# Performance work log

Hardware: AMD Instinct MI355X
Metric: run time of the kernel (lower is better)

Reference implementation:

```python
import jax, jax.numpy as jnp
import numpy as np
from jax import lax

VOCAB = 32000; D = 1024; NL = 4; DI = 2048; S = 16; R = 64; DC = 4
B = 1; L = 1024; EPS = 1e-5


def setup_inputs() -> dict:
    key = jax.random.key(0)
    ks = jax.random.split(key, 16)
    def n(k, shape, s=0.02):
        return jax.random.normal(k, shape, dtype=jnp.float32) * s
    return dict(
        tokens=jax.random.randint(ks[0], (B, L), 0, VOCAB),
        embed=n(ks[1], (VOCAB, D)),
        norm_w=jnp.ones((NL, D), jnp.float32) + n(ks[2], (NL, D)),
        in_proj_w=n(ks[3], (NL, 2 * DI, D)),
        conv_w=n(ks[4], (NL, DI, DC), 0.1),
        conv_b=n(ks[5], (NL, DI)),
        x_proj_w=n(ks[6], (NL, R + 2 * S, DI)),
        dt_proj_w=n(ks[7], (NL, DI, R), 0.1),
        dt_proj_b=n(ks[8], (NL, DI), 0.5),
        A_log=n(ks[9], (NL, DI, S), 0.5),
        D_param=jnp.ones((NL, DI), jnp.float32) + n(ks[10], (NL, DI)),
        out_proj_w=n(ks[11], (NL, D, DI)),
        norm_f_w=jnp.ones((D,), jnp.float32),
        lm_head_w=n(ks[12], (VOCAB, D)),
    )


def _rmsnorm(x, w):
    return x * lax.rsqrt(jnp.mean(x * x, axis=-1, keepdims=True) + EPS) * w


def _mamba_block(x, norm_w, in_w, cw, cb, xw, dtw, dtb, a_log, dp, ow):
    # x: [B, L, D]
    res = x
    x = _rmsnorm(x, norm_w)
    xz = jnp.einsum('bld,ed->ble', x, in_w)      # [B, L, 2*DI]
    u, z = xz[..., :DI], xz[..., DI:]
    # depthwise causal conv over time
    u = jnp.swapaxes(u, 1, 2)                    # [B, DI, L]
    u = lax.conv_general_dilated(u, cw[:, None, :], (1,), [(DC - 1, 0)],
                                 feature_group_count=DI,
                                 dimension_numbers=('NCH', 'OIH', 'NCH'))
    u = jax.nn.silu(u + cb[None, :, None])
    u = jnp.swapaxes(u, 1, 2)                    # [B, L, DI]
    # input-dependent SSM params
    dbc = jnp.einsum('bld,ed->ble', u, xw)       # [B, L, R+2S]
    dt = jax.nn.softplus(jnp.einsum('blr,dr->bld', dbc[..., :R], dtw) + dtb)
    Bm = dbc[..., R:R + S]                       # [B, L, S]
    Cm = dbc[..., R + S:]                        # [B, L, S]
    A = -jnp.exp(a_log)                          # [DI, S]
    dA = jnp.exp(dt[..., None] * A)              # [B, L, DI, S]
    dBu = (dt * u)[..., None] * Bm[:, :, None, :]  # [B, L, DI, S]
    # selective scan over time
    def step(h, inp):
        a_t, b_t, c_t = inp
        h = a_t * h + b_t                        # [B, DI, S]
        y = jnp.einsum('bds,bs->bd', h, c_t)
        return h, y
    h0 = jnp.zeros((x.shape[0], DI, S), x.dtype)
    _, ys = lax.scan(step, h0, (jnp.moveaxis(dA, 1, 0), jnp.moveaxis(dBu, 1, 0), jnp.moveaxis(Cm, 1, 0)))
    y = jnp.moveaxis(ys, 0, 1) + u * dp          # [B, L, DI]
    y = y * jax.nn.silu(z)
    return res + jnp.einsum('bld,od->blo', y, ow)


def reference(tokens, embed, norm_w, in_proj_w, conv_w, conv_b, x_proj_w,
              dt_proj_w, dt_proj_b, A_log, D_param, out_proj_w, norm_f_w, lm_head_w):
    x = embed[tokens]                            # [B, L, D]
    for i in range(NL):
        x = _mamba_block(x, norm_w[i], in_proj_w[i], conv_w[i], conv_b[i],
                         x_proj_w[i], dt_proj_w[i], dt_proj_b[i], A_log[i],
                         D_param[i], out_proj_w[i])
    x = _rmsnorm(x, norm_f_w)
    return jnp.einsum('bld,vd->blv', x, lm_head_w)  # [B, L, VOCAB]
```

## Files before the change

### kernel.cpp

```cpp
#include <hip/hip_runtime.h>
#include <hip/hip_bf16.h>
#include <math.h>


typedef __attribute__((ext_vector_type(8))) short bf16x8;
typedef __attribute__((ext_vector_type(4))) float f32x4;

__device__ __forceinline__ short f2bf(float f) {
  union { float f; unsigned u; } v; v.f = f;
  unsigned u = v.u;
  unsigned r = (u + 0x7FFFu + ((u >> 16) & 1u)) >> 16;
  return (short)r;
}

__device__ __forceinline__ float bf2f(short x) {
  union { unsigned u; float f; } v;
  v.u = ((unsigned)(unsigned short)x) << 16;
  return v.f;
}

__device__ __forceinline__ bf16x8 pack8(float4 a, float4 b) {
  bf16x8 r;
  r[0] = f2bf(a.x); r[1] = f2bf(a.y); r[2] = f2bf(a.z); r[3] = f2bf(a.w);
  r[4] = f2bf(b.x); r[5] = f2bf(b.y); r[6] = f2bf(b.z); r[7] = f2bf(b.w);
  return r;
}

__device__ __forceinline__ unsigned cvtpk(float lo, float hi) {
  unsigned r;
  asm("v_cvt_pk_bf16_f32 %0, %1, %2" : "=v"(r) : "v"(lo), "v"(hi));
  return r;
}

__device__ __forceinline__ float softplus_f(float x) {
  return (x > 20.f) ? x : log1pf(__expf(x));
}

__device__ __forceinline__ void gl_lds16(const void* g, void* l) {
  void* gnc = (void*)g;
  __builtin_amdgcn_global_load_lds((__attribute__((address_space(1))) void*)gnc,
                                   (__attribute__((address_space(3))) void*)l, 16, 0, 0);
}

__global__ __launch_bounds__(256) void cvt5_k(const float* __restrict__ s0, unsigned short* __restrict__ d0, int nb0,
                                              const float* __restrict__ s1, unsigned short* __restrict__ d1, int nb1,
                                              const float* __restrict__ s2, unsigned short* __restrict__ d2, int nb2,
                                              const float* __restrict__ s3, unsigned short* __restrict__ d3, int nb3,
                                              const float* __restrict__ s4, unsigned short* __restrict__ d4) {
  int b = blockIdx.x;
  const float* s; unsigned short* d; int lb;
  if (b < nb0) { s = s0; d = d0; lb = b; }
  else if (b < nb0 + nb1) { s = s1; d = d1; lb = b - nb0; }
  else if (b < nb0 + nb1 + nb2) { s = s2; d = d2; lb = b - nb0 - nb1; }
  else if (b < nb0 + nb1 + nb2 + nb3) { s = s3; d = d3; lb = b - nb0 - nb1 - nb2; }
  else { s = s4; d = d4; lb = b - nb0 - nb1 - nb2 - nb3; }
  size_t base = (size_t)lb * 1024;
#pragma unroll
  for (int u = 0; u < 4; ++u) {
    size_t idx = base + u * 256 + threadIdx.x;
    const float4* p = (const float4*)(s + idx * 8);
    float4 a = p[0], bq = p[1];
    uint4 w;
    w.x = cvtpk(a.x, a.y); w.y = cvtpk(a.z, a.w);
    w.z = cvtpk(bq.x, bq.y); w.w = cvtpk(bq.z, bq.w);
    *(uint4*)(d + idx * 8) = w;
  }
}

__global__ __launch_bounds__(256) void embed_rms_k(const int* __restrict__ tok,
                                                   const float* __restrict__ emb,
                                                   const float* __restrict__ w,
                                                   float* __restrict__ x,
                                                   unsigned short* __restrict__ xn16) {
  int l = blockIdx.x;
  int t = tok[l];
  float4 v = ((const float4*)(emb + (size_t)t * 1024))[threadIdx.x];
  ((float4*)(x + (size_t)l * 1024))[threadIdx.x] = v;
  float ss = v.x * v.x + v.y * v.y + v.z * v.z + v.w * v.w;
  ss += __shfl_down(ss, 32); ss += __shfl_down(ss, 16); ss += __shfl_down(ss, 8);
  ss += __shfl_down(ss, 4);  ss += __shfl_down(ss, 2);  ss += __shfl_down(ss, 1);
  __shared__ float wsum[4];
  if ((threadIdx.x & 63) == 0) wsum[threadIdx.x >> 6] = ss;
  __syncthreads();
  float tot = wsum[0] + wsum[1] + wsum[2] + wsum[3];
  float sc = rsqrtf(tot * (1.0f / 1024.0f) + 1e-5f);
  float4 wv = ((const float4*)w)[threadIdx.x];
  ushort4 o;
  o.x = (unsigned short)f2bf(v.x * sc * wv.x);
  o.y = (unsigned short)f2bf(v.y * sc * wv.y);
  o.z = (unsigned short)f2bf(v.z * sc * wv.z);
  o.w = (unsigned short)f2bf(v.w * sc * wv.w);
  *(ushort4*)(xn16 + (size_t)l * 1024 + threadIdx.x * 4) = o;
}

__global__ __launch_bounds__(256) void reduce_op_rms_k(const float* __restrict__ Cp,
                                                       float* __restrict__ x,
                                                       const float* __restrict__ w,
                                                       unsigned short* __restrict__ y16) {
  int l = blockIdx.x;
  int i = l * 256 + threadIdx.x;
  const float4* p0 = (const float4*)Cp;
  const float4* p1 = (const float4*)(Cp + 1048576);
  const float4* p2 = (const float4*)(Cp + 2097152);
  const float4* p3 = (const float4*)(Cp + 3145728);
  float4 a = p0[i], b = p1[i], c = p2[i], d = p3[i];
  float4 xv = ((float4*)x)[i];
  xv.x += a.x + b.x + c.x + d.x;
  xv.y += a.y + b.y + c.y + d.y;
  xv.z += a.z + b.z + c.z + d.z;
  xv.w += a.w + b.w + c.w + d.w;
  ((float4*)x)[i] = xv;
  float ss = xv.x * xv.x + xv.y * xv.y + xv.z * xv.z + xv.w * xv.w;
  ss += __shfl_down(ss, 32); ss += __shfl_down(ss, 16); ss += __shfl_down(ss, 8);
  ss += __shfl_down(ss, 4);  ss += __shfl_down(ss, 2);  ss += __shfl_down(ss, 1);
  __shared__ float wsum[4];
  if ((threadIdx.x & 63) == 0) wsum[threadIdx.x >> 6] = ss;
  __syncthreads();
  float tot = wsum[0] + wsum[1] + wsum[2] + wsum[3];
  float sc = rsqrtf(tot * (1.0f / 1024.0f) + 1e-5f);
  float4 wv = ((const float4*)w)[threadIdx.x];
  ushort4 o;
  o.x = (unsigned short)f2bf(xv.x * sc * wv.x);
  o.y = (unsigned short)f2bf(xv.y * sc * wv.y);
  o.z = (unsigned short)f2bf(xv.z * sc * wv.z);
  o.w = (unsigned short)f2bf(xv.w * sc * wv.w);
  *(ushort4*)(y16 + (size_t)l * 1024 + threadIdx.x * 4) = o;
}

__global__ __launch_bounds__(256) void rmsnorm_k(const float* __restrict__ x,
                                                 const float* __restrict__ w,
                                                 float* __restrict__ y) {
  int l = blockIdx.x;
  const float4* xr = (const float4*)(x + (size_t)l * 1024);
  float4 v = xr[threadIdx.x];
  float ss = v.x * v.x + v.y * v.y + v.z * v.z + v.w * v.w;
  ss += __shfl_down(ss, 32); ss += __shfl_down(ss, 16); ss += __shfl_down(ss, 8);
  ss += __shfl_down(ss, 4);  ss += __shfl_down(ss, 2);  ss += __shfl_down(ss, 1);
  __shared__ float wsum[4];
  if ((threadIdx.x & 63) == 0) wsum[threadIdx.x >> 6] = ss;
  __syncthreads();
  float tot = wsum[0] + wsum[1] + wsum[2] + wsum[3];
  float sc = rsqrtf(tot * (1.0f / 1024.0f) + 1e-5f);
  float4 wv = ((const float4*)w)[threadIdx.x];
  float4 o;
  o.x = v.x * sc * wv.x; o.y = v.y * sc * wv.y;
  o.z = v.z * sc * wv.z; o.w = v.w * sc * wv.w;
  ((float4*)(y + (size_t)l * 1024))[threadIdx.x] = o;
}

__global__ __launch_bounds__(256) void conv_silu_k(const float* __restrict__ xz,
                                                   const float* __restrict__ cw,
                                                   const float* __restrict__ cb,
                                                   float* __restrict__ u,
                                                   unsigned short* __restrict__ u16) {
  int idx = blockIdx.x * 256 + threadIdx.x;
  int d = idx & 2047;
  int l = idx >> 11;
  float acc = cb[d];
#pragma unroll
  for (int j = 0; j < 4; ++j) {
    int ll = l - 3 + j;
    if (ll >= 0) acc = fmaf(xz[(size_t)ll * 4096 + d], cw[d * 4 + j], acc);
  }
  float sig = 1.0f / (1.0f + __expf(-acc));
  float v = acc * sig;
  u[idx] = v;
  if (u16) u16[idx] = (unsigned short)f2bf(v);
}

__global__ __launch_bounds__(256) void gemm16_k(const unsigned short* __restrict__ A, int lda,
                                                const unsigned short* __restrict__ W, int ldw,
                                                const float* __restrict__ addsrc,
                                                const float* __restrict__ spbias,
                                                float* __restrict__ C, int ldc,
                                                unsigned short* __restrict__ C16,
                                                int gx, int N, int K) {
  int total = gridDim.x;
  int lin = blockIdx.x;
  int q = total >> 3, r = total & 7;
  int xcd = lin & 7, idx = lin >> 3;
  int nl = (xcd < r ? xcd * (q + 1) : r * (q + 1) + (xcd - r) * q) + idx;
  const int bm = (nl % gx) << 7;
  const int bn = (nl / gx) << 7;

  const int tid = threadIdx.x;
  const int wid = tid >> 6;
  const int lane = tid & 63;
  const int wm = (wid >> 1) << 6;
  const int wn = (wid & 1) << 6;
  const int fr = lane & 15;
  const int kg = lane >> 4;
  const int srow = lane >> 3;
  const int sch  = lane & 7;
  const int xch  = sch ^ srow;

  __shared__ unsigned short sA[2][8192];
  __shared__ unsigned short sB[2][8192];

  f32x4 acc[4][4];
#pragma unroll
  for (int i = 0; i < 4; ++i)
#pragma unroll
    for (int j = 0; j < 4; ++j) acc[i][j] = (f32x4){0.f, 0.f, 0.f, 0.f};

  auto STAGE = [&](int b, int k0) {
#pragma unroll
    for (int t = 0; t < 4; ++t) {
      int g = (wid << 2) + t;
      int row = (g << 3) + srow;
      const unsigned short* ga = A + (size_t)(bm + row) * lda + k0 + (xch << 3);
      int wrow = bn + row; if (wrow >= N) wrow = N - 1;
      const unsigned short* gw = W + (size_t)wrow * ldw + k0 + (xch << 3);
      gl_lds16(ga, &sA[b][g << 9]);
      gl_lds16(gw, &sB[b][g << 9]);
    }
  };

  auto COMPUTE = [&](int b) {
#pragma unroll
    for (int ks = 0; ks < 2; ++ks) {
      bf16x8 af[4], bw[4];
#pragma unroll
      for (int mi = 0; mi < 4; ++mi) {
        int row = wm + (mi << 4) + fr;
        int xc = ((ks << 2) + kg) ^ (fr & 7);
        af[mi] = *(const bf16x8*)&sA[b][(row << 6) + (xc << 3)];
      }
#pragma unroll
      for (int ni = 0; ni < 4; ++ni) {
        int row = wn + (ni << 4) + fr;
        int xc = ((ks << 2) + kg) ^ (fr & 7);
        bw[ni] = *(const bf16x8*)&sB[b][(row << 6) + (xc << 3)];
      }
#pragma unroll
      for (int mi = 0; mi < 4; ++mi)
#pragma unroll
        for (int ni = 0; ni < 4; ++ni)
          acc[mi][ni] = __builtin_amdgcn_mfma_f32_16x16x32_bf16(af[mi], bw[ni], acc[mi][ni], 0, 0, 0);
    }
  };

  const int nt = K >> 6;
  STAGE(0, 0);
  int cur = 0;
  for (int t = 0; t + 1 < nt; ++t) {
    STAGE(cur ^ 1, (t + 1) << 6);
    asm volatile("s_waitcnt vmcnt(8)" ::: "memory");
    __builtin_amdgcn_s_barrier();
    __builtin_amdgcn_sched_barrier(0);
    COMPUTE(cur);
    __builtin_amdgcn_s_barrier();
    cur ^= 1;
  }
  asm volatile("s_waitcnt vmcnt(0)" ::: "memory");
  __builtin_amdgcn_s_barrier();
  __builtin_amdgcn_sched_barrier(0);
  COMPUTE(cur);

#pragma unroll
  for (int mi = 0; mi < 4; ++mi)
#pragma unroll
    for (int ni = 0; ni < 4; ++ni) {
      int n = bn + wn + (ni << 4) + fr;
      if (n < N) {
#pragma unroll
        for (int i = 0; i < 4; ++i) {
          int m = bm + wm + (mi << 4) + (kg << 2) + i;
          size_t off = (size_t)m * ldc + n;
          float v = acc[mi][ni][i];
          if (addsrc) v += addsrc[off];
          if (spbias) v = softplus_f(v + spbias[n]);
          C[off] = v;
          if (C16) C16[off] = (unsigned short)f2bf(v);
        }
      }
    }
}

__global__ __launch_bounds__(256) void gemm16sk_k(const unsigned short* __restrict__ A, int lda,
                                                  const unsigned short* __restrict__ W, int ldw,
                                                  float* __restrict__ Cp, int ldc,
                                                  int gx, int N, int Kchunk, int Mtot) {
  int total = gridDim.x;
  int lin = blockIdx.x;
  int q = total >> 3, r = total & 7;
  int xcd = lin & 7, idx = lin >> 3;
  int nl = (xcd < r ? xcd * (q + 1) : r * (q + 1) + (xcd - r) * q) + idx;
  const int bm = (nl % gx) << 7;
  const int bn = (nl / gx) << 7;
  const int ksplit = blockIdx.y;
  const int kbase = ksplit * Kchunk;

  const int tid = threadIdx.x;
  const int wid = tid >> 6;
  const int lane = tid & 63;
  const int wm = (wid >> 1) << 6;
  const int wn = (wid & 1) << 6;
  const int fr = lane & 15;
  const int kg = lane >> 4;
  const int srow = lane >> 3;
  const int sch  = lane & 7;
  const int xch  = sch ^ srow;

  __shared__ unsigned short sA[2][8192];
  __shared__ unsigned short sB[2][8192];

  f32x4 acc[4][4];
#pragma unroll
  for (int i = 0; i < 4; ++i)
#pragma unroll
    for (int j = 0; j < 4; ++j) acc[i][j] = (f32x4){0.f, 0.f, 0.f, 0.f};

  auto STAGE = [&](int b, int k0) {
#pragma unroll
    for (int t = 0; t < 4; ++t) {
      int g = (wid << 2) + t;
      int row = (g << 3) + srow;
      const unsigned short* ga = A + (size_t)(bm + row) * lda + k0 + (xch << 3);
      int wrow = bn + row; if (wrow >= N) wrow = N - 1;
      const unsigned short* gw = W + (size_t)wrow * ldw + k0 + (xch << 3);
      gl_lds16(ga, &sA[b][g << 9]);
      gl_lds16(gw, &sB[b][g << 9]);
    }
  };

  auto COMPUTE = [&](int b) {
#pragma unroll
    for (int ks = 0; ks < 2; ++ks) {
      bf16x8 af[4], bw[4];
#pragma unroll
      for (int mi = 0; mi < 4; ++mi) {
        int row = wm + (mi << 4) + fr;
        int xc = ((ks << 2) + kg) ^ (fr & 7);
        af[mi] = *(const bf16x8*)&sA[b][(row << 6) + (xc << 3)];
      }
#pragma unroll
      for (int ni = 0; ni < 4; ++ni) {
        int row = wn + (ni << 4) + fr;
        int xc = ((ks << 2) + kg) ^ (fr & 7);
        bw[ni] = *(const bf16x8*)&sB[b][(row << 6) + (xc << 3)];
      }
#pragma unroll
      for (int mi = 0; mi < 4; ++mi)
#pragma unroll
        for (int ni = 0; ni < 4; ++ni)
          acc[mi][ni] = __builtin_amdgcn_mfma_f32_16x16x32_bf16(af[mi], bw[ni], acc[mi][ni], 0, 0, 0);
    }
  };

  const int nt = Kchunk >> 6;
  STAGE(0, kbase);
  int cur = 0;
  for (int t = 0; t + 1 < nt; ++t) {
    STAGE(cur ^ 1, kbase + ((t + 1) << 6));
    asm volatile("s_waitcnt vmcnt(8)" ::: "memory");
    __builtin_amdgcn_s_barrier();
    __builtin_amdgcn_sched_barrier(0);
    COMPUTE(cur);
    __builtin_amdgcn_s_barrier();
    cur ^= 1;
  }
  asm volatile("s_waitcnt vmcnt(0)" ::: "memory");
  __builtin_amdgcn_s_barrier();
  __builtin_amdgcn_sched_barrier(0);
  COMPUTE(cur);

  float* Cs = Cp + (size_t)ksplit * Mtot * ldc;
#pragma unroll
  for (int mi = 0; mi < 4; ++mi)
#pragma unroll
    for (int ni = 0; ni < 4; ++ni) {
      int n = bn + wn + (ni << 4) + fr;
      if (n < N) {
#pragma unroll
        for (int i = 0; i < 4; ++i) {
          int m = bm + wm + (mi << 4) + (kg << 2) + i;
          Cs[(size_t)m * ldc + n] = acc[mi][ni][i];
        }
      }
    }
}

__global__ __launch_bounds__(256) void reduce_xp_k(const float* __restrict__ Cp,
                                                   float* __restrict__ dbc,
                                                   unsigned short* __restrict__ dbc16) {
  int i = blockIdx.x * 256 + threadIdx.x;
  float v = Cp[i] + Cp[98304 + i] + Cp[2 * 98304 + i] + Cp[3 * 98304 + i];
  dbc[i] = v;
  dbc16[i] = (unsigned short)f2bf(v);
}

__global__ __launch_bounds__(512, 2) void gemm_lm_k(const unsigned short* __restrict__ A, int lda,
                                                    const unsigned short* __restrict__ W, int ldw,
                                                    float* __restrict__ C, int ldc,
                                                    int gx, int N, int K) {
  int total = gridDim.x;
  int lin = blockIdx.x;
  int q = total >> 3, r = total & 7;
  int xcd = lin & 7, idx = lin >> 3;
  int nl = (xcd < r ? xcd * (q + 1) : r * (q + 1) + (xcd - r) * q) + idx;
  const int bm = (nl % gx) << 7;
  const int bn = (nl / gx) << 8;

  const int tid = threadIdx.x;
  const int wid = tid >> 6;
  const int lane = tid & 63;
  const int wm = (wid >> 2) << 6;
  const int wn = (wid & 3) << 6;
  const int fr = lane & 15;
  const int kg = lane >> 4;
  const int srow = lane >> 3;
  const int sch  = lane & 7;
  const int xch  = sch ^ srow;

  __shared__ unsigned short sA[3][8192];
  __shared__ unsigned short sB[3][16384];

  f32x4 acc[4][4];
#pragma unroll
  for (int i = 0; i < 4; ++i)
#pragma unroll
    for (int j = 0; j < 4; ++j) acc[i][j] = (f32x4){0.f, 0.f, 0.f, 0.f};

  auto STAGE = [&](int b, int t) {
    int k0 = t << 6;
#pragma unroll
    for (int i = 0; i < 6; ++i) {
      int g = wid * 6 + i;
      if (g < 16) {
        int row = (g << 3) + srow;
        const unsigned short* ga = A + (size_t)(bm + row) * lda + k0 + (xch << 3);
        gl_lds16(ga, &sA[b][g << 9]);
      } else {
        int gb = g - 16;
        int row = (gb << 3) + srow;
        int wrow = bn + row; if (wrow >= N) wrow = N - 1;
        const unsigned short* gw = W + (size_t)wrow * ldw + k0 + (xch << 3);
        gl_lds16(gw, &sB[b][gb << 9]);
      }
    }
  };

  auto COMPUTE = [&](int b) {
#pragma unroll
    for (int ks = 0; ks < 2; ++ks) {
      bf16x8 af[4], bw[4];
#pragma unroll
      for (int mi = 0; mi < 4; ++mi) {
        int row = wm + (mi << 4) + fr;
        int xc = ((ks << 2) + kg) ^ (fr & 7);
        af[mi] = *(const bf16x8*)&sA[b][(row << 6) + (xc << 3)];
      }
#pragma unroll
      for (int ni = 0; ni < 4; ++ni) {
        int row = wn + (ni << 4) + fr;
        int xc = ((ks << 2) + kg) ^ (fr & 7);
        bw[ni] = *(const bf16x8*)&sB[b][(row << 6) + (xc << 3)];
      }
#pragma unroll
      for (int mi = 0; mi < 4; ++mi)
#pragma unroll
        for (int ni = 0; ni < 4; ++ni)
          acc[mi][ni] = __builtin_amdgcn_mfma_f32_16x16x32_bf16(af[mi], bw[ni], acc[mi][ni], 0, 0, 0);
    }
  };

  const int nt = K >> 6;
  STAGE(0, 0); STAGE(1, 1); STAGE(2, 2);

  int bi = 0;
  for (int t = 0; t <= nt - 3; ++t) {
    asm volatile("s_waitcnt vmcnt(12)" ::: "memory");
    __builtin_amdgcn_s_barrier();
    __builtin_amdgcn_sched_barrier(0);
    COMPUTE(bi);
    __builtin_amdgcn_s_barrier();
    if (t + 3 < nt) STAGE(bi, t + 3);
    bi = (bi == 2) ? 0 : bi + 1;
  }
  asm volatile("s_waitcnt vmcnt(6)" ::: "memory");
  __builtin_amdgcn_s_barrier();
  __builtin_amdgcn_sched_barrier(0);
  COMPUTE(bi);
  __builtin_amdgcn_s_barrier();
  bi = (bi == 2) ? 0 : bi + 1;
  asm volatile("s_waitcnt vmcnt(0)" ::: "memory");
  __builtin_amdgcn_s_barrier();
  __builtin_amdgcn_sched_barrier(0);
  COMPUTE(bi);

#pragma unroll
  for (int mi = 0; mi < 4; ++mi)
#pragma unroll
    for (int ni = 0; ni < 4; ++ni) {
      int n = bn + wn + (ni << 4) + fr;
      if (n < N) {
#pragma unroll
        for (int i = 0; i < 4; ++i) {
          int m = bm + wm + (mi << 4) + (kg << 2) + i;
          C[(size_t)m * ldc + n] = acc[mi][ni][i];
        }
      }
    }
}

__global__ __launch_bounds__(256) void gemm_bt_k(const float* __restrict__ A, int lda,
                                                 const float* __restrict__ W, int ldw,
                                                 const float* __restrict__ addsrc,
                                                 float* __restrict__ C, int ldc,
                                                 int N, int K) {
  const int tid  = threadIdx.x;
  const int srow = tid >> 1;
  const int skg  = (tid & 1) << 1;
  const int bm = blockIdx.x << 7;
  const int bn = blockIdx.y << 7;
  const int wid = tid >> 6;
  const int lane = tid & 63;
  const int wm = (wid >> 1) << 6;
  const int wn = (wid & 1) << 6;
  const int fr = lane & 15;
  const int kg = lane >> 4;

  __shared__ bf16x8 lA[4][128];
  __shared__ bf16x8 lB[4][128];

  f32x4 zero4 = {0.f, 0.f, 0.f, 0.f};
  f32x4 acc[4][4];
#pragma unroll
  for (int i = 0; i < 4; ++i)
#pragma unroll
    for (int j = 0; j < 4; ++j) acc[i][j] = zero4;

  const bool wvalid = (bn + srow) < N;
  const float* gA = A + (size_t)(bm + srow) * lda + (skg << 3);
  const float* gW = W + (size_t)(wvalid ? (bn + srow) : 0) * ldw + (skg << 3);

  for (int k0 = 0; k0 < K; k0 += 32) {
    float4 a0 = *(const float4*)(gA + k0);
    float4 a1 = *(const float4*)(gA + k0 + 4);
    float4 a2 = *(const float4*)(gA + k0 + 8);
    float4 a3 = *(const float4*)(gA + k0 + 12);
    float4 w0 = make_float4(0.f, 0.f, 0.f, 0.f), w1 = w0, w2 = w0, w3 = w0;
    if (wvalid) {
      w0 = *(const float4*)(gW + k0);
      w1 = *(const float4*)(gW + k0 + 4);
      w2 = *(const float4*)(gW + k0 + 8);
      w3 = *(const float4*)(gW + k0 + 12);
    }
    __syncthreads();
    lA[skg][srow]     = pack8(a0, a1);
    lA[skg + 1][srow] = pack8(a2, a3);
    lB[skg][srow]     = pack8(w0, w1);
    lB[skg + 1][srow] = pack8(w2, w3);
    __syncthreads();

    bf16x8 af[4], bf_[4];
#pragma unroll
    for (int mi = 0; mi < 4; ++mi) af[mi] = lA[kg][wm + (mi << 4) + fr];
#pragma unroll
    for (int ni = 0; ni < 4; ++ni) bf_[ni] = lB[kg][wn + (ni << 4) + fr];
#pragma unroll
    for (int mi = 0; mi < 4; ++mi)
#pragma unroll
      for (int ni = 0; ni < 4; ++ni)
        acc[mi][ni] = __builtin_amdgcn_mfma_f32_16x16x32_bf16(af[mi], bf_[ni], acc[mi][ni], 0, 0, 0);
  }

#pragma unroll
  for (int mi = 0; mi < 4; ++mi)
#pragma unroll
    for (int ni = 0; ni < 4; ++ni) {
      int n = bn + wn + (ni << 4) + fr;
      if (n < N) {
#pragma unroll
        for (int i = 0; i < 4; ++i) {
          int m = bm + wm + (mi << 4) + (kg << 2) + i;
          size_t off = (size_t)m * ldc + n;
          float v = acc[mi][ni][i];
          if (addsrc) v += addsrc[off];
          C[off] = v;
        }
      }
    }
}

#define NCH 32
#define CHL 32
#define SDP 68

__global__ __launch_bounds__(256) void scan_p1f_k(const unsigned short* __restrict__ dbc16,
                                                  const unsigned short* __restrict__ dtw16,
                                                  const float* __restrict__ dtb,
                                                  const float* __restrict__ u,
                                                  const float* __restrict__ dbc,
                                                  const float* __restrict__ A_log,
                                                  float* __restrict__ Pg,
                                                  float* __restrict__ qg) {
  int tid = threadIdx.x;
  int s = tid & 15, dg = tid >> 4;
  int d0 = blockIdx.x << 4;
  int d = d0 + dg;
  int c = blockIdx.y;
  int l0 = c << 5;

  __shared__ float sdbc[32][SDP];
  __shared__ float sdtw[16][SDP];
  __shared__ float sdt[32][16];

  {
    int row = tid >> 3, ch = tid & 7;
    bf16x8 v = *(const bf16x8*)&dbc16[(size_t)(l0 + row) * 96 + ch * 8];
#pragma unroll
    for (int j = 0; j < 8; ++j) sdbc[row][ch * 8 + j] = bf2f(v[j]);
    if (tid < 128) {
      bf16x8 w = *(const bf16x8*)&dtw16[(size_t)(d0 + row) * 64 + ch * 8];
#pragma unroll
      for (int j = 0; j < 8; ++j) sdtw[row][ch * 8 + j] = bf2f(w[j]);
    }
  }
  __syncthreads();
  {
    int ll = tid >> 4, dd = tid & 15;
    float a0 = 0.f, a1 = 0.f;
#pragma unroll 8
    for (int k = 0; k < 64; ++k) {
      float wv = sdtw[dd][k];
      a0 = fmaf(sdbc[ll][k], wv, a0);
      a1 = fmaf(sdbc[ll + 16][k], wv, a1);
    }
    float bias = dtb[d0 + dd];
    sdt[ll][dd]      = softplus_f(a0 + bias);
    sdt[ll + 16][dd] = softplus_f(a1 + bias);
  }
  __syncthreads();

  float A = -__expf(A_log[d * 16 + s]);
  float P = 1.f, q = 0.f;
#pragma unroll 4
  for (int i = 0; i < CHL; ++i) {
    int l = l0 + i;
    float dt = sdt[i][dg];
    float dA = __expf(dt * A);
    P *= dA;
    q = fmaf(dA, q, dt * u[(size_t)l * 2048 + d] * dbc[l * 96 + 64 + s]);
  }
  size_t o = (size_t)c * 32768 + d * 16 + s;
  Pg[o] = P;
  qg[o] = q;
}

__global__ __launch_bounds__(256) void scan_p3f_k(const unsigned short* __restrict__ dbc16,
                                                  const unsigned short* __restrict__ dtw16,
                                                  const float* __restrict__ dtb,
                                                  const float* __restrict__ u,
                                                  const float* __restrict__ dbc,
                                                  const float* __restrict__ xz,
                                                  const float* __restrict__ A_log,
                                                  const float* __restrict__ Dp,
                                                  const float* __restrict__ Pg,
                                                  const float* __restrict__ qg,
                                                  unsigned short* __restrict__ y16) {
  int tid = threadIdx.x;
  int s = tid & 15, dg = tid >> 4;
  int d0 = blockIdx.x << 4;
  int d = d0 + dg;
  int c = blockIdx.y;
  int l0 = c << 5;

  __shared__ float sdbc[32][SDP];
  __shared__ float sdtw[16][SDP];
  __shared__ float sdt[32][16];

  {
    int row = tid >> 3, ch = tid & 7;
    bf16x8 v = *(const bf16x8*)&dbc16[(size_t)(l0 + row) * 96 + ch * 8];
#pragma unroll
    for (int j = 0; j < 8; ++j) sdbc[row][ch * 8 + j] = bf2f(v[j]);
    if (tid < 128) {
      bf16x8 w = *(const bf16x8*)&dtw16[(size_t)(d0 + row) * 64 + ch * 8];
#pragma unroll
      for (int j = 0; j < 8; ++j) sdtw[row][ch * 8 + j] = bf2f(w[j]);
    }
  }
  __syncthreads();
  {
    int ll = tid >> 4, dd = tid & 15;
    float a0 = 0.f, a1 = 0.f;
#pragma unroll 8
    for (int k = 0; k < 64; ++k) {
      float wv = sdtw[dd][k];
      a0 = fmaf(sdbc[ll][k], wv, a0);
      a1 = fmaf(sdbc[ll + 16][k], wv, a1);
    }
    float bias = dtb[d0 + dd];
    sdt[ll][dd]      = softplus_f(a0 + bias);
    sdt[ll + 16][dd] = softplus_f(a1 + bias);
  }
  __syncthreads();

  float A = -__expf(A_log[d * 16 + s]);
  float dpar = Dp[d];
  float h = 0.f;
  for (int cc = 0; cc < c; ++cc) {
    size_t o = (size_t)cc * 32768 + d * 16 + s;
    h = fmaf(Pg[o], h, qg[o]);
  }
#pragma unroll 4
  for (int i = 0; i < CHL; ++i) {
    int l = l0 + i;
    size_t rd = (size_t)l * 2048 + d;
    float dt = sdt[i][dg];
    float uv = u[rd];
    float dA = __expf(dt * A);
    h = fmaf(dA, h, dt * uv * dbc[l * 96 + 64 + s]);
    float p = h * dbc[l * 96 + 80 + s];
    p += __shfl_xor(p, 1); p += __shfl_xor(p, 2);
    p += __shfl_xor(p, 4); p += __shfl_xor(p, 8);
    if (s == 0) {
      float zv = xz[(size_t)l * 4096 + 2048 + d];
      float sig = 1.0f / (1.0f + __expf(-zv));
      y16[rd] = (unsigned short)f2bf((p + uv * dpar) * (zv * sig));
    }
  }
}

__global__ __launch_bounds__(256) void scan_p1_k(const float* __restrict__ dtr,
                                                 const float* __restrict__ u,
                                                 const float* __restrict__ dbc,
                                                 const float* __restrict__ A_log,
                                                 const float* __restrict__ dtb,
                                                 float* __restrict__ Pg,
                                                 float* __restrict__ qg) {
  int tid = threadIdx.x;
  int s = tid & 15, dg = tid >> 4;
  int d = (blockIdx.x << 4) + dg;
  int c = blockIdx.y;
  int l0 = c << 5;
  float A = -__expf(A_log[d * 16 + s]);
  float bias = dtb[d];
  float P = 1.f, q = 0.f;
#pragma unroll 4
  for (int i = 0; i < CHL; ++i) {
    int l = l0 + i;
    float dt = softplus_f(dtr[(size_t)l * 2048 + d] + bias);
    float dA = __expf(dt * A);
    P *= dA;
    q = fmaf(dA, q, dt * u[(size_t)l * 2048 + d] * dbc[l * 96 + 64 + s]);
  }
  size_t o = (size_t)c * 32768 + d * 16 + s;
  Pg[o] = P;
  qg[o] = q;
}

__global__ __launch_bounds__(256) void scan_p2_k(const float* __restrict__ Pg,
                                                 const float* __restrict__ qg,
                                                 float* __restrict__ hst) {
  int idx = blockIdx.x * 256 + threadIdx.x;
  float h = 0.f;
#pragma unroll
  for (int c = 0; c < NCH; ++c) {
    size_t o = (size_t)c * 32768 + idx;
    hst[o] = h;
    h = fmaf(Pg[o], h, qg[o]);
  }
}

__global__ __launch_bounds__(256) void scan_p3_k(const float* __restrict__ dtr,
                                                 const float* __restrict__ u,
                                                 const float* __restrict__ dbc,
                                                 const float* __restrict__ xz,
                                                 const float* __restrict__ A_log,
                                                 const float* __restrict__ Dp,
                                                 const float* __restrict__ dtb,
                                                 const float* __restrict__ hst,
                                                 float* __restrict__ y) {
  int tid = threadIdx.x;
  int s = tid & 15, dg = tid >> 4;
  int d = (blockIdx.x << 4) + dg;
  int c = blockIdx.y;
  int l0 = c << 5;
  float A = -__expf(A_log[d * 16 + s]);
  float dpar = Dp[d];
  float bias = dtb[d];
  float h = hst[(size_t)c * 32768 + d * 16 + s];
#pragma unroll 4
  for (int i = 0; i < CHL; ++i) {
    int l = l0 + i;
    size_t rd = (size_t)l * 2048 + d;
    float dt = softplus_f(dtr[rd] + bias);
    float uv = u[rd];
    float dA = __expf(dt * A);
    h = fmaf(dA, h, dt * uv * dbc[l * 96 + 64 + s]);
    float p = h * dbc[l * 96 + 80 + s];
    p += __shfl_xor(p, 1); p += __shfl_xor(p, 2);
    p += __shfl_xor(p, 4); p += __shfl_xor(p, 8);
    if (s == 0) {
      float zv = xz[(size_t)l * 4096 + 2048 + d];
      float sig = 1.0f / (1.0f + __expf(-zv));
      y[rd] = (p + uv * dpar) * (zv * sig);
    }
  }
}

extern "C" void kernel_launch(void* const* d_in, const int* in_sizes, int n_in,
                              void* d_out, int out_size, void* d_ws, size_t ws_size,
                              hipStream_t stream) {
  const int*   tokens = (const int*)d_in[0];
  const float* embed  = (const float*)d_in[1];
  const float* norm_w = (const float*)d_in[2];
  const float* in_w   = (const float*)d_in[3];
  const float* conv_w = (const float*)d_in[4];
  const float* conv_b = (const float*)d_in[5];
  const float* x_w    = (const float*)d_in[6];
  const float* dt_w   = (const float*)d_in[7];
  const float* dt_b   = (const float*)d_in[8];
  const float* A_log  = (const float*)d_in[9];
  const float* D_par  = (const float*)d_in[10];
  const float* out_w  = (const float*)d_in[11];
  const float* normf  = (const float*)d_in[12];
  const float* lm_w   = (const float*)d_in[13];

  float* out = (float*)d_out;
  float* x    = out;
  float* xz   = x    + 1024 * 1024;
  float* u    = xz   + 1024 * 4096;
  float* dtv  = u    + 1024 * 2048;
  float* dbc  = dtv  + 1024 * 2048;
  float* Pg   = dbc  + 1024 * 96;
  float* qg   = Pg   + 32 * 32768;
  float* hst  = qg   + 32 * 32768;
  float* xn_f = hst  + 32 * 32768;
  float* y_f  = xn_f + 1024 * 1024;
  unsigned short* xn16  = (unsigned short*)(y_f + 1024 * 2048);
  unsigned short* u16   = xn16 + 1024 * 1024;
  unsigned short* y16   = u16  + 1024 * 2048;
  unsigned short* dbc16 = y16  + 1024 * 2048;
  float* part_op = (float*)(dbc16 + 1024 * 96);
  float* part_xp = part_op + 4 * 1048576;

  unsigned short* inw16 = (unsigned short*)d_ws;
  unsigned short* oww16 = inw16 + 16777216;
  unsigned short* xw16  = oww16 + 8388608;
  unsigned short* dtw16 = xw16  + 786432;
  unsigned short* lmw16 = dtw16 + 524288;
  unsigned short* xnf16 = lmw16 + 32768000;
  const size_t need = (size_t)(16777216 + 8388608 + 786432 + 524288 + 32768000 + 1048576) * 2;
  const bool fast = ws_size >= need;

  if (fast) {
    cvt5_k<<<7232, 256, 0, stream>>>(in_w, inw16, 2048,
                                     out_w, oww16, 1024,
                                     x_w, xw16, 96,
                                     dt_w, dtw16, 64,
                                     lm_w, lmw16);
    embed_rms_k<<<1024, 256, 0, stream>>>(tokens, embed, norm_w, x, xn16);

    for (int i = 0; i < 4; ++i) {
      gemm16_k<<<256, 256, 0, stream>>>(xn16, 1024, inw16 + (size_t)i * 4194304, 1024,
                                        nullptr, nullptr, xz, 4096, nullptr, 8, 4096, 1024);
      conv_silu_k<<<8192, 256, 0, stream>>>(xz, conv_w + i * 8192, conv_b + i * 2048, u, u16);
      gemm16sk_k<<<dim3(8, 4), 256, 0, stream>>>(u16, 2048, xw16 + (size_t)i * 196608, 2048,
                                                 part_xp, 96, 8, 96, 512, 1024);
      reduce_xp_k<<<384, 256, 0, stream>>>(part_xp, dbc, dbc16);
      scan_p1f_k<<<dim3(128, NCH), 256, 0, stream>>>(dbc16, dtw16 + (size_t)i * 131072,
                                                     dt_b + i * 2048, u, dbc,
                                                     A_log + i * 32768, Pg, qg);
      scan_p3f_k<<<dim3(128, NCH), 256, 0, stream>>>(dbc16, dtw16 + (size_t)i * 131072,
                                                     dt_b + i * 2048, u, dbc, xz,
                                                     A_log + i * 32768, D_par + i * 2048,
                                                     Pg, qg, y16);
      gemm16sk_k<<<dim3(64, 4), 256, 0, stream>>>(y16, 2048, oww16 + (size_t)i * 2097152, 2048,
                                                  part_op, 1024, 8, 1024, 512, 1024);
      const float* wn = (i < 3) ? (norm_w + (i + 1) * 1024) : normf;
      unsigned short* yn = (i < 3) ? xn16 : xnf16;
      reduce_op_rms_k<<<1024, 256, 0, stream>>>(part_op, x, wn, yn);
    }

    gemm_lm_k<<<1000, 512, 0, stream>>>(xnf16, 1024, lmw16, 1024, out, 32000, 8, 32000, 1024);
  } else {
    float* xnf_f = (float*)d_ws;
    embed_rms_k<<<1024, 256, 0, stream>>>(tokens, embed, norm_w, x, xn16);
    for (int i = 0; i < 4; ++i) {
      rmsnorm_k<<<1024, 256, 0, stream>>>(x, norm_w + i * 1024, xn_f);
      gemm_bt_k<<<dim3(8, 32), 256, 0, stream>>>(xn_f, 1024, in_w + (size_t)i * 4194304, 1024,
                                                 nullptr, xz, 4096, 4096, 1024);
      conv_silu_k<<<8192, 256, 0, stream>>>(xz, conv_w + i * 8192, conv_b + i * 2048, u, nullptr);
      gemm_bt_k<<<dim3(8, 1), 256, 0, stream>>>(u, 2048, x_w + (size_t)i * 196608, 2048,
                                                nullptr, dbc, 96, 96, 2048);
      gemm_bt_k<<<dim3(8, 16), 256, 0, stream>>>(dbc, 96, dt_w + (size_t)i * 131072, 64,
                                                 nullptr, dtv, 2048, 2048, 64);
      scan_p1_k<<<dim3(128, NCH), 256, 0, stream>>>(dtv, u, dbc, A_log + i * 32768,
                                                    dt_b + i * 2048, Pg, qg);
      scan_p2_k<<<128, 256, 0, stream>>>(Pg, qg, hst);
      scan_p3_k<<<dim3(128, NCH), 256, 0, stream>>>(dtv, u, dbc, xz, A_log + i * 32768,
                                                    D_par + i * 2048, dt_b + i * 2048, hst, y_f);
      gemm_bt_k<<<dim3(8, 8), 256, 0, stream>>>(y_f, 2048, out_w + (size_t)i * 2097152, 2048,
                                                x, x, 1024, 1024, 2048);
    }
    rmsnorm_k<<<1024, 256, 0, stream>>>(x, normf, xnf_f);
    gemm_bt_k<<<dim3(8, 250), 256, 0, stream>>>(xnf_f, 1024, lm_w, 1024,
                                                nullptr, out, 32000, 32000, 1024);
  }
}
```

Measured before the change: 894.3 us.

## Fuse lm_head bf16 conversion into GEMM, fold xproj reduce into scans, deepen out_proj split-K

The LM-head GEMM now reads fp32 weights directly, converts them to bf16 in registers and writes them to LDS. This removes the separate conversion pass over the 32000x1024 weight and its bf16 round-trip through memory. The reduce_xp kernel is dropped, and the scan kernels sum the four split-K partials of x_proj themselves, keeping dbc in fp32 shared memory. The out_proj split-K is doubled to 8 slices, with the residual reduce summing 8 partials. In exchange the LM GEMM pipeline gets more complex, with register staging and two B buffers. Each scan block also repeats the partial sum, and the residual reduce reads more partial traffic.

```diff
diff --git a/kernel.cpp b/kernel.cpp
--- a/kernel.cpp
+++ b/kernel.cpp
@@ -42,18 +42,16 @@
                                    (__attribute__((address_space(3))) void*)l, 16, 0, 0);
 }
 
-__global__ __launch_bounds__(256) void cvt5_k(const float* __restrict__ s0, unsigned short* __restrict__ d0, int nb0,
+__global__ __launch_bounds__(256) void cvt4_k(const float* __restrict__ s0, unsigned short* __restrict__ d0, int nb0,
                                               const float* __restrict__ s1, unsigned short* __restrict__ d1, int nb1,
                                               const float* __restrict__ s2, unsigned short* __restrict__ d2, int nb2,
-                                              const float* __restrict__ s3, unsigned short* __restrict__ d3, int nb3,
-                                              const float* __restrict__ s4, unsigned short* __restrict__ d4) {
+                                              const float* __restrict__ s3, unsigned short* __restrict__ d3, int nb3) {
   int b = blockIdx.x;
   const float* s; unsigned short* d; int lb;
   if (b < nb0) { s = s0; d = d0; lb = b; }
   else if (b < nb0 + nb1) { s = s1; d = d1; lb = b - nb0; }
   else if (b < nb0 + nb1 + nb2) { s = s2; d = d2; lb = b - nb0 - nb1; }
-  else if (b < nb0 + nb1 + nb2 + nb3) { s = s3; d = d3; lb = b - nb0 - nb1 - nb2; }
-  else { s = s4; d = d4; lb = b - nb0 - nb1 - nb2 - nb3; }
+  else { s = s3; d = d3; lb = b - nb0 - nb1 - nb2; }
   size_t base = (size_t)lb * 1024;
 #pragma unroll
   for (int u = 0; u < 4; ++u) {
@@ -99,16 +97,14 @@
                                                        unsigned short* __restrict__ y16) {
   int l = blockIdx.x;
   int i = l * 256 + threadIdx.x;
-  const float4* p0 = (const float4*)Cp;
-  const float4* p1 = (const float4*)(Cp + 1048576);
-  const float4* p2 = (const float4*)(Cp + 2097152);
-  const float4* p3 = (const float4*)(Cp + 3145728);
-  float4 a = p0[i], b = p1[i], c = p2[i], d = p3[i];
+  float4 acc = make_float4(0.f, 0.f, 0.f, 0.f);
+#pragma unroll
+  for (int s = 0; s < 8; ++s) {
+    float4 p = ((const float4*)(Cp + (size_t)s * 1048576))[i];
+    acc.x += p.x; acc.y += p.y; acc.z += p.z; acc.w += p.w;
+  }
   float4 xv = ((float4*)x)[i];
-  xv.x += a.x + b.x + c.x + d.x;
-  xv.y += a.y + b.y + c.y + d.y;
-  xv.z += a.z + b.z + c.z + d.z;
-  xv.w += a.w + b.w + c.w + d.w;
+  xv.x += acc.x; xv.y += acc.y; xv.z += acc.z; xv.w += acc.w;
   ((float4*)x)[i] = xv;
   float ss = xv.x * xv.x + xv.y * xv.y + xv.z * xv.z + xv.w * xv.w;
   ss += __shfl_down(ss, 32); ss += __shfl_down(ss, 16); ss += __shfl_down(ss, 8);
@@ -390,10 +386,10 @@
   dbc16[i] = (unsigned short)f2bf(v);
 }
 
-__global__ __launch_bounds__(512, 2) void gemm_lm_k(const unsigned short* __restrict__ A, int lda,
-                                                    const unsigned short* __restrict__ W, int ldw,
-                                                    float* __restrict__ C, int ldc,
-                                                    int gx, int N, int K) {
+__global__ __launch_bounds__(512, 2) void gemm_lmf_k(const unsigned short* __restrict__ A, int lda,
+                                                     const float* __restrict__ W, int ldw,
+                                                     float* __restrict__ C, int ldc,
+                                                     int gx, int N, int K) {
   int total = gridDim.x;
   int lin = blockIdx.x;
   int q = total >> 3, r = total & 7;
@@ -413,8 +409,13 @@
   const int sch  = lane & 7;
   const int xch  = sch ^ srow;
 
+  const int wr_row  = tid >> 1;
+  const int wr_half = tid & 1;
+  int wr_grow = bn + wr_row; if (wr_grow >= N) wr_grow = N - 1;
+  const float* gWrow = W + (size_t)wr_grow * ldw + wr_half * 32;
+
   __shared__ unsigned short sA[3][8192];
-  __shared__ unsigned short sB[3][16384];
+  __shared__ unsigned short sB[2][16384];
 
   f32x4 acc[4][4];
 #pragma unroll
@@ -422,26 +423,56 @@
 #pragma unroll
     for (int j = 0; j < 4; ++j) acc[i][j] = (f32x4){0.f, 0.f, 0.f, 0.f};
 
-  auto STAGE = [&](int b, int t) {
+  float4 wrA[8], wrB[8];
+
+  auto STAGE_A = [&](unsigned short* buf, int t) {
     int k0 = t << 6;
 #pragma unroll
-    for (int i = 0; i < 6; ++i) {
-      int g = wid * 6 + i;
-      if (g < 16) {
-        int row = (g << 3) + srow;
-        const unsigned short* ga = A + (size_t)(bm + row) * lda + k0 + (xch << 3);
-        gl_lds16(ga, &sA[b][g << 9]);
-      } else {
-        int gb = g - 16;
-        int row = (gb << 3) + srow;
-        int wrow = bn + row; if (wrow >= N) wrow = N - 1;
-        const unsigned short* gw = W + (size_t)wrow * ldw + k0 + (xch << 3);
-        gl_lds16(gw, &sB[b][gb << 9]);
-      }
+    for (int i = 0; i < 2; ++i) {
+      int g = (wid << 1) + i;
+      int row = (g << 3) + srow;
+      const unsigned short* ga = A + (size_t)(bm + row) * lda + k0 + (xch << 3);
+      gl_lds16(ga, &buf[g << 9]);
     }
   };
 
-  auto COMPUTE = [&](int b) {
+  auto WLOAD_A = [&](int t) {
+    const float4* p = (const float4*)(gWrow + (t << 6));
+#pragma unroll
+    for (int j = 0; j < 8; ++j) wrA[j] = p[j];
+  };
+  auto WLOAD_B = [&](int t) {
+    const float4* p = (const float4*)(gWrow + (t << 6));
+#pragma unroll
+    for (int j = 0; j < 8; ++j) wrB[j] = p[j];
+  };
+
+  auto WWRITE_A = [&](unsigned short* buf) {
+#pragma unroll
+    for (int c2 = 0; c2 < 4; ++c2) {
+      int c = (wr_half << 2) + c2;
+      uint4 val;
+      val.x = cvtpk(wrA[2 * c2].x,     wrA[2 * c2].y);
+      val.y = cvtpk(wrA[2 * c2].z,     wrA[2 * c2].w);
+      val.z = cvtpk(wrA[2 * c2 + 1].x, wrA[2 * c2 + 1].y);
+      val.w = cvtpk(wrA[2 * c2 + 1].z, wrA[2 * c2 + 1].w);
+      *(uint4*)&buf[(wr_row << 6) + ((c ^ (wr_row & 7)) << 3)] = val;
+    }
+  };
+  auto WWRITE_B = [&](unsigned short* buf) {
+#pragma unroll
+    for (int c2 = 0; c2 < 4; ++c2) {
+      int c = (wr_half << 2) + c2;
+      uint4 val;
+      val.x = cvtpk(wrB[2 * c2].x,     wrB[2 * c2].y);
+      val.y = cvtpk(wrB[2 * c2].z,     wrB[2 * c2].w);
+      val.z = cvtpk(wrB[2 * c2 + 1].x, wrB[2 * c2 + 1].y);
+      val.w = cvtpk(wrB[2 * c2 + 1].z, wrB[2 * c2 + 1].w);
+      *(uint4*)&buf[(wr_row << 6) + ((c ^ (wr_row & 7)) << 3)] = val;
+    }
+  };
+
+  auto COMPUTE = [&](const unsigned short* bufa, const unsigned short* bufb) {
 #pragma unroll
     for (int ks = 0; ks < 2; ++ks) {
       bf16x8 af[4], bw[4];
@@ -449,13 +480,13 @@
       for (int mi = 0; mi < 4; ++mi) {
         int row = wm + (mi << 4) + fr;
         int xc = ((ks << 2) + kg) ^ (fr & 7);
-        af[mi] = *(const bf16x8*)&sA[b][(row << 6) + (xc << 3)];
+        af[mi] = *(const bf16x8*)&bufa[(row << 6) + (xc << 3)];
       }
 #pragma unroll
       for (int ni = 0; ni < 4; ++ni) {
         int row = wn + (ni << 4) + fr;
         int xc = ((ks << 2) + kg) ^ (fr & 7);
-        bw[ni] = *(const bf16x8*)&sB[b][(row << 6) + (xc << 3)];
+        bw[ni] = *(const bf16x8*)&bufb[(row << 6) + (xc << 3)];
       }
 #pragma unroll
       for (int mi = 0; mi < 4; ++mi)
@@ -466,28 +497,42 @@
   };
 
   const int nt = K >> 6;
-  STAGE(0, 0); STAGE(1, 1); STAGE(2, 2);
-
-  int bi = 0;
-  for (int t = 0; t <= nt - 3; ++t) {
-    asm volatile("s_waitcnt vmcnt(12)" ::: "memory");
+
+  STAGE_A(sA[0], 0); WLOAD_A(0);
+  STAGE_A(sA[1], 1); WLOAD_B(1);
+  __builtin_amdgcn_sched_barrier(0);
+  asm volatile("s_waitcnt vmcnt(10)" ::: "memory");
+  __builtin_amdgcn_sched_barrier(0);
+  WWRITE_A(sB[0]);
+  STAGE_A(sA[2], 2); WLOAD_A(2);
+  __builtin_amdgcn_sched_barrier(0);
+  asm volatile("s_waitcnt lgkmcnt(0)" ::: "memory");
+  __builtin_amdgcn_s_barrier();
+
+  for (int t = 0; t < nt; ++t) {
+    int rr = t % 3;
+    int b = t & 1;
+    COMPUTE(sA[rr], sB[b]);
     __builtin_amdgcn_s_barrier();
-    __builtin_amdgcn_sched_barrier(0);
-    COMPUTE(bi);
-    __builtin_amdgcn_s_barrier();
-    if (t + 3 < nt) STAGE(bi, t + 3);
-    bi = (bi == 2) ? 0 : bi + 1;
-  }
-  asm volatile("s_waitcnt vmcnt(6)" ::: "memory");
-  __builtin_amdgcn_s_barrier();
-  __builtin_amdgcn_sched_barrier(0);
-  COMPUTE(bi);
-  __builtin_amdgcn_s_barrier();
-  bi = (bi == 2) ? 0 : bi + 1;
-  asm volatile("s_waitcnt vmcnt(0)" ::: "memory");
-  __builtin_amdgcn_s_barrier();
-  __builtin_amdgcn_sched_barrier(0);
-  COMPUTE(bi);
+    if (t + 1 < nt) {
+      if (t + 2 < nt) {
+        asm volatile("s_waitcnt vmcnt(10)" ::: "memory");
+      } else {
+        asm volatile("s_waitcnt vmcnt(0)" ::: "memory");
+      }
+      __builtin_amdgcn_sched_barrier(0);
+      if (((t + 1) & 1) == 0) {
+        WWRITE_A(sB[b ^ 1]);
+        if (t + 3 < nt) { STAGE_A(sA[rr], t + 3); WLOAD_A(t + 3); }
+      } else {
+        WWRITE_B(sB[b ^ 1]);
+        if (t + 3 < nt) { STAGE_A(sA[rr], t + 3); WLOAD_B(t + 3); }
+      }
+      __builtin_amdgcn_sched_barrier(0);
+      asm volatile("s_waitcnt lgkmcnt(0)" ::: "memory");
+      __builtin_amdgcn_s_barrier();
+    }
+  }
 
 #pragma unroll
   for (int mi = 0; mi < 4; ++mi)
@@ -588,11 +633,10 @@
 #define CHL 32
 #define SDP 68
 
-__global__ __launch_bounds__(256) void scan_p1f_k(const unsigned short* __restrict__ dbc16,
+__global__ __launch_bounds__(256) void scan_p1f_k(const float* __restrict__ part_xp,
                                                   const unsigned short* __restrict__ dtw16,
                                                   const float* __restrict__ dtb,
                                                   const float* __restrict__ u,
-                                                  const float* __restrict__ dbc,
                                                   const float* __restrict__ A_log,
                                                   float* __restrict__ Pg,
                                                   float* __restrict__ qg) {
@@ -603,16 +647,20 @@
   int c = blockIdx.y;
   int l0 = c << 5;
 
-  __shared__ float sdbc[32][SDP];
+  __shared__ float sdbc[32][100];
   __shared__ float sdtw[16][SDP];
   __shared__ float sdt[32][16];
 
   {
-    int row = tid >> 3, ch = tid & 7;
-    bf16x8 v = *(const bf16x8*)&dbc16[(size_t)(l0 + row) * 96 + ch * 8];
-#pragma unroll
-    for (int j = 0; j < 8; ++j) sdbc[row][ch * 8 + j] = bf2f(v[j]);
+#pragma unroll
+    for (int it = 0; it < 12; ++it) {
+      int idx = it * 256 + tid;
+      int row = idx / 96, col = idx - row * 96;
+      size_t g = (size_t)(l0 + row) * 96 + col;
+      sdbc[row][col] = part_xp[g] + part_xp[98304 + g] + part_xp[2 * 98304 + g] + part_xp[3 * 98304 + g];
+    }
     if (tid < 128) {
+      int row = tid >> 3, ch = tid & 7;
       bf16x8 w = *(const bf16x8*)&dtw16[(size_t)(d0 + row) * 64 + ch * 8];
 #pragma unroll
       for (int j = 0; j < 8; ++j) sdtw[row][ch * 8 + j] = bf2f(w[j]);
@@ -642,18 +690,17 @@
     float dt = sdt[i][dg];
     float dA = __expf(dt * A);
     P *= dA;
-    q = fmaf(dA, q, dt * u[(size_t)l * 2048 + d] * dbc[l * 96 + 64 + s]);
+    q = fmaf(dA, q, dt * u[(size_t)l * 2048 + d] * sdbc[i][64 + s]);
   }
   size_t o = (size_t)c * 32768 + d * 16 + s;
   Pg[o] = P;
   qg[o] = q;
 }
 
-__global__ __launch_bounds__(256) void scan_p3f_k(const unsigned short* __restrict__ dbc16,
+__global__ __launch_bounds__(256) void scan_p3f_k(const float* __restrict__ part_xp,
                                                   const unsigned short* __restrict__ dtw16,
                                                   const float* __restrict__ dtb,
                                                   const float* __restrict__ u,
-                                                  const float* __restrict__ dbc,
                                                   const float* __restrict__ xz,
                                                   const float* __restrict__ A_log,
                                                   const float* __restrict__ Dp,
@@ -667,16 +714,20 @@
   int c = blockIdx.y;
   int l0 = c << 5;
 
-  __shared__ float sdbc[32][SDP];
+  __shared__ float sdbc[32][100];
   __shared__ float sdtw[16][SDP];
   __shared__ float sdt[32][16];
 
   {
-    int row = tid >> 3, ch = tid & 7;
-    bf16x8 v = *(const bf16x8*)&dbc16[(size_t)(l0 + row) * 96 + ch * 8];
-#pragma unroll
-    for (int j = 0; j < 8; ++j) sdbc[row][ch * 8 + j] = bf2f(v[j]);
+#pragma unroll
+    for (int it = 0; it < 12; ++it) {
+      int idx = it * 256 + tid;
+      int row = idx / 96, col = idx - row * 96;
+      size_t g = (size_t)(l0 + row) * 96 + col;
+      sdbc[row][col] = part_xp[g] + part_xp[98304 + g] + part_xp[2 * 98304 + g] + part_xp[3 * 98304 + g];
+    }
     if (tid < 128) {
+      int row = tid >> 3, ch = tid & 7;
       bf16x8 w = *(const bf16x8*)&dtw16[(size_t)(d0 + row) * 64 + ch * 8];
 #pragma unroll
       for (int j = 0; j < 8; ++j) sdtw[row][ch * 8 + j] = bf2f(w[j]);
@@ -712,8 +763,8 @@
     float dt = sdt[i][dg];
     float uv = u[rd];
     float dA = __expf(dt * A);
-    h = fmaf(dA, h, dt * uv * dbc[l * 96 + 64 + s]);
-    float p = h * dbc[l * 96 + 80 + s];
+    h = fmaf(dA, h, dt * uv * sdbc[i][64 + s]);
+    float p = h * sdbc[i][80 + s];
     p += __shfl_xor(p, 1); p += __shfl_xor(p, 2);
     p += __shfl_xor(p, 4); p += __shfl_xor(p, 8);
     if (s == 0) {
@@ -836,23 +887,21 @@
   unsigned short* y16   = u16  + 1024 * 2048;
   unsigned short* dbc16 = y16  + 1024 * 2048;
   float* part_op = (float*)(dbc16 + 1024 * 96);
-  float* part_xp = part_op + 4 * 1048576;
+  float* part_xp = part_op + 8 * 1048576;
 
   unsigned short* inw16 = (unsigned short*)d_ws;
   unsigned short* oww16 = inw16 + 16777216;
   unsigned short* xw16  = oww16 + 8388608;
   unsigned short* dtw16 = xw16  + 786432;
-  unsigned short* lmw16 = dtw16 + 524288;
-  unsigned short* xnf16 = lmw16 + 32768000;
-  const size_t need = (size_t)(16777216 + 8388608 + 786432 + 524288 + 32768000 + 1048576) * 2;
+  unsigned short* xnf16 = dtw16 + 524288;
+  const size_t need = (size_t)(16777216 + 8388608 + 786432 + 524288 + 1048576) * 2;
   const bool fast = ws_size >= need;
 
   if (fast) {
-    cvt5_k<<<7232, 256, 0, stream>>>(in_w, inw16, 2048,
+    cvt4_k<<<3232, 256, 0, stream>>>(in_w, inw16, 2048,
                                      out_w, oww16, 1024,
                                      x_w, xw16, 96,
-                                     dt_w, dtw16, 64,
-                                     lm_w, lmw16);
+                                     dt_w, dtw16, 64);
     embed_rms_k<<<1024, 256, 0, stream>>>(tokens, embed, norm_w, x, xn16);
 
     for (int i = 0; i < 4; ++i) {
@@ -861,22 +910,21 @@
       conv_silu_k<<<8192, 256, 0, stream>>>(xz, conv_w + i * 8192, conv_b + i * 2048, u, u16);
       gemm16sk_k<<<dim3(8, 4), 256, 0, stream>>>(u16, 2048, xw16 + (size_t)i * 196608, 2048,
                                                  part_xp, 96, 8, 96, 512, 1024);
-      reduce_xp_k<<<384, 256, 0, stream>>>(part_xp, dbc, dbc16);
-      scan_p1f_k<<<dim3(128, NCH), 256, 0, stream>>>(dbc16, dtw16 + (size_t)i * 131072,
-                                                     dt_b + i * 2048, u, dbc,
+      scan_p1f_k<<<dim3(128, NCH), 256, 0, stream>>>(part_xp, dtw16 + (size_t)i * 131072,
+                                                     dt_b + i * 2048, u,
                                                      A_log + i * 32768, Pg, qg);
-      scan_p3f_k<<<dim3(128, NCH), 256, 0, stream>>>(dbc16, dtw16 + (size_t)i * 131072,
-                                                     dt_b + i * 2048, u, dbc, xz,
+      scan_p3f_k<<<dim3(128, NCH), 256, 0, stream>>>(part_xp, dtw16 + (size_t)i * 131072,
+                                                     dt_b + i * 2048, u, xz,
                                                      A_log + i * 32768, D_par + i * 2048,
                                                      Pg, qg, y16);
-      gemm16sk_k<<<dim3(64, 4), 256, 0, stream>>>(y16, 2048, oww16 + (size_t)i * 2097152, 2048,
-                                                  part_op, 1024, 8, 1024, 512, 1024);
+      gemm16sk_k<<<dim3(64, 8), 256, 0, stream>>>(y16, 2048, oww16 + (size_t)i * 2097152, 2048,
+                                                  part_op, 1024, 8, 1024, 256, 1024);
       const float* wn = (i < 3) ? (norm_w + (i + 1) * 1024) : normf;
       unsigned short* yn = (i < 3) ? xn16 : xnf16;
       reduce_op_rms_k<<<1024, 256, 0, stream>>>(part_op, x, wn, yn);
     }
 
-    gemm_lm_k<<<1000, 512, 0, stream>>>(xnf16, 1024, lmw16, 1024, out, 32000, 8, 32000, 1024);
+    gemm_lmf_k<<<1000, 512, 0, stream>>>(xnf16, 1024, lm_w, 1024, out, 32000, 8, 32000, 1024);
   } else {
     float* xnf_f = (float*)d_ws;
     embed_rms_k<<<1024, 256, 0, stream>>>(tokens, embed, norm_w, x, xn16);
```

After: 1.001 ms. +11.9%, slower.
